# Optimization experiments

Measured on AMD Instinct MI355X. Metric: run time of the kernel, lower is better.

## Reference

```python
import jax, jax.numpy as jnp
import numpy as np

D_MODEL = 1024
N_HEADS = 16
D_V = D_MODEL // N_HEADS  # 64; o_proj maps d_model -> d_v (quirk of the source)
B, S = 4, 2048


def setup_inputs() -> dict:
    key = jax.random.key(0)
    ks = jax.random.split(key, 5)
    scale = 1.0 / np.sqrt(D_MODEL)
    return {
        "in_features": jax.random.normal(ks[0], (B, S, D_MODEL), dtype=jnp.float32),
        "Wq": jax.random.normal(ks[1], (D_MODEL, D_MODEL), dtype=jnp.float32) * scale,
        "Wk": jax.random.normal(ks[2], (D_MODEL, D_MODEL), dtype=jnp.float32) * scale,
        "Wv": jax.random.normal(ks[3], (D_MODEL, D_MODEL), dtype=jnp.float32) * scale,
        "Wo": jax.random.normal(ks[4], (D_V, D_MODEL), dtype=jnp.float32) * scale,
    }


def reference(in_features, Wq, Wk, Wv, Wo):
    # Linear(in, out): y = x @ W^T, no bias. NOTE: source never splits heads;
    # attention runs single-head over the full d_model dims.
    Q = jnp.einsum('bsd,ed->bse', in_features, Wq)  # [B,S,D]
    K = jnp.einsum('bsd,ed->bse', in_features, Wk)
    V = jnp.einsum('bsd,ed->bse', in_features, Wv)

    scores = jnp.einsum('bqd,bkd->bqk', Q, K)       # [B,S,S]
    causal = jnp.tril(jnp.ones((S, S), dtype=bool))  # True = keep
    # source applies -inf mask BEFORE scaling (equivalent result)
    scores = jnp.where(causal[None, :, :], scores, -jnp.inf)
    scores = scores / jnp.sqrt(jnp.float32(D_MODEL))  # K.size(-1) == d_model
    attn = jax.nn.softmax(scores, axis=-1)
    ctx = jnp.einsum('bqk,bkd->bqd', attn, V)        # [B,S,D]
    return jnp.einsum('bsd,vd->bsv', ctx, Wo)        # [B,S,D_V]
```

## Files before the change

### kernel.cpp

```cpp
#include <hip/hip_runtime.h>
#include <math.h>

typedef unsigned short u16;
typedef unsigned int u32;
typedef __attribute__((ext_vector_type(8))) short short8;
typedef __attribute__((ext_vector_type(4))) short short4v;
typedef __attribute__((ext_vector_type(4))) float f32x4;

#define BB 4
#define SS 2048
#define DD 1024
#define DV 64
#define NYU 1152
#define BS (BB * SS)
#define SCALE (1.0f / 32.0f)

__device__ __forceinline__ u16 f2bf(float f) {
    u32 u = __builtin_bit_cast(u32, f);
    u32 r = u + 0x7fffu + ((u >> 16) & 1u);
    return (u16)(r >> 16);
}
__device__ __forceinline__ float bf2f(u16 b) {
    return __builtin_bit_cast(float, (u32)b << 16);
}
__device__ __forceinline__ void storeC(float* p, float v) { *p = v; }
__device__ __forceinline__ void storeC(u16* p, float v) { *p = f2bf(v); }

__global__ __launch_bounds__(256) void prep(const float* __restrict__ x,
                                            const float* __restrict__ Wq,
                                            const float* __restrict__ Wk,
                                            const float* __restrict__ Wo,
                                            const float* __restrict__ Wv,
                                            u16* __restrict__ x16,
                                            u16* __restrict__ Wqt,
                                            u16* __restrict__ Wkt,
                                            float* __restrict__ wpart,
                                            float* __restrict__ out,
                                            float* __restrict__ Lacc) {
    __shared__ float smem[64 * 128];
    const int b = blockIdx.x;
    const int tid = threadIdx.x;
    if (b < 64) {
        const int bb = b;
        const int echunk = (bb & 7) * 128;
        const int kc = bb >> 3, kbase = kc * 128;
        for (int idx = tid; idx < 64 * 128; idx += 256)
            smem[idx] = Wo[(size_t)(idx >> 7) * DD + kbase + (idx & 127)];
        __syncthreads();
        const int eo = echunk + (tid & 31) * 4;
        const int ob = (tid >> 5) * 8;
        float acc[8][4] = {};
        for (int k = 0; k < 128; ++k) {
            f32x4 wv = *(const f32x4*)&Wv[(size_t)(kbase + k) * DD + eo];
#pragma unroll
            for (int oi = 0; oi < 8; ++oi) {
                float s = smem[(ob + oi) * 128 + k];
                acc[oi][0] += s * wv.x; acc[oi][1] += s * wv.y;
                acc[oi][2] += s * wv.z; acc[oi][3] += s * wv.w;
            }
        }
#pragma unroll
        for (int oi = 0; oi < 8; ++oi)
            *(f32x4*)&wpart[((size_t)kc * 64 + ob + oi) * DD + eo] =
                (f32x4){acc[oi][0], acc[oi][1], acc[oi][2], acc[oi][3]};
    } else if (b < 576) {
        const int bb = b - 64;
        const float* src = (bb >> 8) ? Wk : Wq;
        u16* dst = (bb >> 8) ? Wkt : Wqt;
        const int rem = bb & 255;
        const int e0 = (rem >> 4) * 64, d0 = (rem & 15) * 64;
        u16* t = (u16*)smem;
        const int g = tid >> 6, lane = tid & 63;
        for (int r = g; r < 64; r += 4)
            t[r * 72 + lane] = f2bf(src[(size_t)(e0 + r) * DD + d0 + lane]);
        __syncthreads();
        for (int r = g; r < 64; r += 4)
            dst[(size_t)(d0 + r) * DD + e0 + lane] = t[lane * 72 + r];
    } else if (b < 8768) {
        int i = (b - 576) * 256 + tid;
        f32x4 v = ((const f32x4*)x)[i];
        short4v o;
        o.x = (short)f2bf(v.x); o.y = (short)f2bf(v.y);
        o.z = (short)f2bf(v.z); o.w = (short)f2bf(v.w);
        ((short4v*)x16)[i] = o;
    } else if (b < 9280) {
        int i = (b - 8768) * 256 + tid;
        ((f32x4*)out)[i] = (f32x4){0.f, 0.f, 0.f, 0.f};
    } else {
        int i = (b - 9280) * 256 + tid;
        ((f32x4*)Lacc)[i] = (f32x4){0.f, 0.f, 0.f, 0.f};
    }
}

__global__ __launch_bounds__(256) void reduce_all(const float* __restrict__ Gpart,
                                                  const float* __restrict__ wpart,
                                                  u16* __restrict__ Wall2) {
    const int bx = blockIdx.x;
    const int e0 = threadIdx.x * 4;
    f32x4 s = (f32x4){0.f, 0.f, 0.f, 0.f};
    if (bx < 1024) {
#pragma unroll
        for (int kc = 0; kc < 4; ++kc)
            s += *(const f32x4*)&Gpart[(size_t)kc * DD * DD + (size_t)bx * DD + e0];
    } else {
#pragma unroll
        for (int kc = 0; kc < 8; ++kc)
            s += *(const f32x4*)&wpart[((size_t)kc * 64 + bx - 1024) * DD + e0];
    }
    short4v ov;
    ov.x = (short)f2bf(s.x); ov.y = (short)f2bf(s.y);
    ov.z = (short)f2bf(s.z); ov.w = (short)f2bf(s.w);
    *(short4v*)&Wall2[(size_t)bx * DD + e0] = ov;
}

template <int TM, int TN, int WM, int WN, typename OutT, int MODE>
__global__ __launch_bounds__(WM * WN * 64) void gemm_nt_mfma(
    const u16* __restrict__ A, const u16* __restrict__ B, OutT* __restrict__ C,
    int lda, int ldb, int ldc, int K, long sA, long sB, long sC,
    u16* __restrict__ Utp) {
    constexpr int NW = WM * WN;
    constexpr int CA = TM / 16;
    constexpr int CB = TN / 16;
    constexpr int RT = TM / WM;
    constexpr int CT = TN / WN;
    constexpr int AI = RT / 16;
    constexpr int AJ = CT / 16;

    const int z = blockIdx.z;
    A += (size_t)z * sA;
    B += (size_t)z * sB;
    C += (size_t)z * sC;
    int m0, n0;
    if constexpr (MODE == 3) {
        const int b = blockIdx.x;
        const int r = b & 7, q = b >> 3;
        constexpr int RPX = 8192 / TM / 8;
        constexpr int NP = 1152 / TN;
        m0 = (r * RPX + q / NP) * TM;
        n0 = (q % NP) * TN;
    } else {
        m0 = blockIdx.y * TM;
        n0 = blockIdx.x * TN;
    }

    __shared__ u16 As[2][TM * 32];
    __shared__ u16 Bs[2][TN * 32];

    const int tid = threadIdx.x;
    const int w = tid >> 6, lane = tid & 63;
    const int wm = w / WN, wn = w % WN;
    const int lrow = lane >> 2;
    const int lcolsw = (((lane & 3) ^ ((lrow >> 1) & 3)) << 3);
    const int m16 = lane & 15;
    const int rdo = (((lane >> 4) ^ ((m16 >> 1) & 3)) << 3);

    f32x4 acc[AI][AJ];
#pragma unroll
    for (int i = 0; i < AI; ++i)
#pragma unroll
        for (int j = 0; j < AJ; ++j) acc[i][j] = (f32x4){0.f, 0.f, 0.f, 0.f};

    auto stage = [&](int t, int bufi) {
        const int k0 = t * 32;
        for (int c = w; c < CA; c += NW) {
            const u16* g = A + (size_t)(m0 + c * 16 + lrow) * lda + k0 + lcolsw;
            __builtin_amdgcn_global_load_lds(
                (const __attribute__((address_space(1))) void*)g,
                (__attribute__((address_space(3))) void*)(&As[bufi][c * 512]), 16, 0, 0);
        }
        for (int c = w; c < CB; c += NW) {
            const u16* g = B + (size_t)(n0 + c * 16 + lrow) * ldb + k0 + lcolsw;
            __builtin_amdgcn_global_load_lds(
                (const __attribute__((address_space(1))) void*)g,
                (__attribute__((address_space(3))) void*)(&Bs[bufi][c * 512]), 16, 0, 0);
        }
    };

    const int nk = K >> 5;
    stage(0, 0);
    asm volatile("s_waitcnt vmcnt(0)" ::: "memory");
    __syncthreads();

    int cur = 0;
    for (int t = 0; t < nk; ++t) {
        if (t + 1 < nk) stage(t + 1, cur ^ 1);

        short8 a[AI], b[AJ];
#pragma unroll
        for (int i = 0; i < AI; ++i)
            a[i] = *(const short8*)&As[cur][(wm * RT + i * 16 + m16) * 32 + rdo];
#pragma unroll
        for (int j = 0; j < AJ; ++j)
            b[j] = *(const short8*)&Bs[cur][(wn * CT + j * 16 + m16) * 32 + rdo];
#pragma unroll
        for (int i = 0; i < AI; ++i)
#pragma unroll
            for (int j = 0; j < AJ; ++j)
                acc[i][j] = __builtin_amdgcn_mfma_f32_16x16x32_bf16(a[i], b[j], acc[i][j], 0, 0, 0);

        if (t + 1 < nk) {
            asm volatile("s_waitcnt vmcnt(0)" ::: "memory");
            __syncthreads();
        }
        cur ^= 1;
    }

    const int crow0 = m0 + wm * RT + (lane >> 4) * 4;
    const int ccol0 = n0 + wn * CT + m16;
#pragma unroll
    for (int i = 0; i < AI; ++i)
#pragma unroll
        for (int j = 0; j < AJ; ++j)
#pragma unroll
            for (int r = 0; r < 4; ++r) {
                const float v = acc[i][j][r];
                storeC(&C[(size_t)(crow0 + i * 16 + r) * ldc + ccol0 + j * 16], v);
                if constexpr (MODE == 3) {
                    if (n0 + wn * CT == 1024)
                        Utp[(size_t)(ccol0 + j * 16 - 1024) * BS + crow0 + i * 16 + r] = f2bf(v);
                }
            }
}

__global__ __launch_bounds__(128) void scores_pv(const u16* __restrict__ YU,
                                                 const u16* __restrict__ x16,
                                                 const u16* __restrict__ Ut,
                                                 float* __restrict__ out,
                                                 float* __restrict__ Lacc) {
    const int b = blockIdx.x;
    const int r8 = b & 7;
    const int z = r8 >> 1;
    const int t = 2 * (b >> 3) + (r8 & 1);
    auto cum = [](int yy) { int h = yy >> 1; return (yy & 1) ? (h + 1) * (h + 1) : h * (h + 1); };
    int y = (int)(2.0f * sqrtf((float)t + 0.25f));
    if (y > 31) y = 31;
    while (y < 31 && cum(y + 1) <= t) ++y;
    while (y > 0 && cum(y) > t) --y;
    const int m0 = y * 64;
    const int n0 = (t - cum(y)) * 128;

    const u16* A = YU + (size_t)z * SS * NYU;
    const u16* B = x16 + (size_t)z * SS * DD;

    __shared__ union ShU {
        struct { u16 As[2][64 * 32]; u16 Bs[2][128 * 32]; } s;
        u16 Ps[64 * 136];
    } sh;

    const int tid = threadIdx.x;
    const int w = tid >> 6, lane = tid & 63;
    const int lrow = lane >> 2;
    const int lcolsw = (((lane & 3) ^ ((lrow >> 1) & 3)) << 3);
    const int m16 = lane & 15;
    const int kh = (lane >> 4) * 8;
    const int rdo = (((lane >> 4) ^ ((m16 >> 1) & 3)) << 3);

    f32x4 acc[4][4];
#pragma unroll
    for (int i = 0; i < 4; ++i)
#pragma unroll
        for (int j = 0; j < 4; ++j) acc[i][j] = (f32x4){0.f, 0.f, 0.f, 0.f};

    auto stage = [&](int tt, int bufi) {
        const int k0 = tt * 32;
        for (int c = w; c < 4; c += 2) {
            const u16* g = A + (size_t)(m0 + c * 16 + lrow) * NYU + k0 + lcolsw;
            __builtin_amdgcn_global_load_lds(
                (const __attribute__((address_space(1))) void*)g,
                (__attribute__((address_space(3))) void*)(&sh.s.As[bufi][c * 512]), 16, 0, 0);
        }
        for (int c = w; c < 8; c += 2) {
            const u16* g = B + (size_t)(n0 + c * 16 + lrow) * DD + k0 + lcolsw;
            __builtin_amdgcn_global_load_lds(
                (const __attribute__((address_space(1))) void*)g,
                (__attribute__((address_space(3))) void*)(&sh.s.Bs[bufi][c * 512]), 16, 0, 0);
        }
    };

    stage(0, 0);
    asm volatile("s_waitcnt vmcnt(0)" ::: "memory");
    __syncthreads();

    int cur = 0;
    for (int tt = 0; tt < 32; ++tt) {
        if (tt + 1 < 32) stage(tt + 1, cur ^ 1);

        short8 a[4], bb[4];
#pragma unroll
        for (int i = 0; i < 4; ++i)
            a[i] = *(const short8*)&sh.s.As[cur][(i * 16 + m16) * 32 + rdo];
#pragma unroll
        for (int j = 0; j < 4; ++j)
            bb[j] = *(const short8*)&sh.s.Bs[cur][(w * 64 + j * 16 + m16) * 32 + rdo];
#pragma unroll
        for (int i = 0; i < 4; ++i)
#pragma unroll
            for (int j = 0; j < 4; ++j)
                acc[i][j] = __builtin_amdgcn_mfma_f32_16x16x32_bf16(a[i], bb[j], acc[i][j], 0, 0, 0);

        if (tt + 1 < 32) {
            asm volatile("s_waitcnt vmcnt(0)" ::: "memory");
            __syncthreads();
        }
        cur ^= 1;
    }
    __syncthreads();

    const int rl0 = (lane >> 4) * 4;
    const int cl0 = w * 64 + m16;
#pragma unroll
    for (int i = 0; i < 4; ++i)
#pragma unroll
        for (int j = 0; j < 4; ++j)
#pragma unroll
            for (int r = 0; r < 4; ++r) {
                const int rl = rl0 + i * 16 + r;
                const int cl = cl0 + j * 16;
                float p = __expf(acc[i][j][r] * SCALE);
                sh.Ps[rl * 136 + cl] = (n0 + cl <= m0 + rl) ? f2bf(p) : (u16)0;
            }
    __syncthreads();

    short8 ones8;
#pragma unroll
    for (int e = 0; e < 8; ++e) ones8[e] = (short)0x3F80;

    const u16* Utz = Ut + (size_t)z * SS + n0;
    f32x4 accO[2][4], accL[2];
#pragma unroll
    for (int i = 0; i < 2; ++i) {
        accL[i] = (f32x4){0.f, 0.f, 0.f, 0.f};
#pragma unroll
        for (int j = 0; j < 4; ++j) accO[i][j] = (f32x4){0.f, 0.f, 0.f, 0.f};
    }
#pragma unroll
    for (int ks = 0; ks < 4; ++ks) {
        const int k0 = ks * 32;
        short8 a[2], bb[4];
#pragma unroll
        for (int i = 0; i < 2; ++i)
            a[i] = *(const short8*)&sh.Ps[(w * 32 + i * 16 + m16) * 136 + k0 + kh];
#pragma unroll
        for (int j = 0; j < 4; ++j)
            bb[j] = *(const short8*)&Utz[(size_t)(j * 16 + m16) * BS + k0 + kh];
#pragma unroll
        for (int i = 0; i < 2; ++i) {
#pragma unroll
            for (int j = 0; j < 4; ++j)
                accO[i][j] = __builtin_amdgcn_mfma_f32_16x16x32_bf16(a[i], bb[j], accO[i][j], 0, 0, 0);
            accL[i] = __builtin_amdgcn_mfma_f32_16x16x32_bf16(a[i], ones8, accL[i], 0, 0, 0);
        }
    }

    float* Oz = out + (size_t)z * SS * DV;
    float* Lz = Lacc + (size_t)z * SS;
    const int wrow = m0 + w * 32 + (lane >> 4) * 4;
#pragma unroll
    for (int i = 0; i < 2; ++i) {
#pragma unroll
        for (int j = 0; j < 4; ++j)
#pragma unroll
            for (int r = 0; r < 4; ++r)
                atomicAdd(&Oz[(size_t)(wrow + i * 16 + r) * DV + j * 16 + m16],
                          accO[i][j][r]);
        if (m16 == 0)
#pragma unroll
            for (int r = 0; r < 4; ++r)
                atomicAdd(&Lz[wrow + i * 16 + r], accL[i][r]);
    }
}

__global__ __launch_bounds__(256) void normalize(float* __restrict__ out,
                                                 const float* __restrict__ Lacc) {
    int i = blockIdx.x * 256 + threadIdx.x;
    f32x4 v = ((f32x4*)out)[i];
    const float inv = 1.f / Lacc[(i * 4) >> 6];
    v.x *= inv; v.y *= inv; v.z *= inv; v.w *= inv;
    ((f32x4*)out)[i] = v;
}

extern "C" void kernel_launch(void* const* d_in, const int* in_sizes, int n_in,
                              void* d_out, int out_size, void* d_ws, size_t ws_size,
                              hipStream_t stream) {
    const float* x  = (const float*)d_in[0];
    const float* Wq = (const float*)d_in[1];
    const float* Wk = (const float*)d_in[2];
    const float* Wv = (const float*)d_in[3];
    const float* Wo = (const float*)d_in[4];
    float* out = (float*)d_out;

    u16* x16   = (u16*)d_ws;
    u16* Wqt16 = x16 + (size_t)BB * SS * DD;
    u16* Wkt16 = Wqt16 + (size_t)DD * DD;
    u16* Wall2 = Wkt16 + (size_t)DD * DD;
    u16* YU    = Wall2 + (size_t)NYU * DD;
    u16* Ut    = YU + (size_t)BB * SS * NYU;
    float* wpart = (float*)(Ut + (size_t)DV * BS);
    float* Lacc  = wpart + (size_t)8 * 64 * DD;
    float* Gpart = (float*)YU;

    prep<<<dim3(9288), 256, 0, stream>>>(x, Wq, Wk, Wo, Wv, x16, Wqt16, Wkt16,
                                         wpart, out, Lacc);

    gemm_nt_mfma<64, 64, 2, 2, float, 0><<<dim3(16, 16, 4), 256, 0, stream>>>(
        Wkt16, Wqt16, Gpart, DD, DD, DD, 256, 256, 256, (long)DD * DD, nullptr);

    reduce_all<<<dim3(1088), 256, 0, stream>>>(Gpart, wpart, Wall2);

    gemm_nt_mfma<64, 128, 1, 2, u16, 3><<<dim3(1152), 128, 0, stream>>>(
        x16, Wall2, YU, DD, DD, NYU, DD, 0, 0, 0, Ut);

    scores_pv<<<dim3(1088), 128, 0, stream>>>(YU, x16, Ut, out, Lacc);

    normalize<<<dim3(out_size / 4 / 256), 256, 0, stream>>>(out, Lacc);
}
```

Baseline: 200.0 us.

## Fuse YU projection GEMM and causal scores kernel with flag-based dataflow sync

Merges the YU/Ut projection GEMM and the causal scores+PV kernel into one persistent-style launch. Producer blocks signal per-panel completion through global atomic flags, and consumer blocks spin until their row and column panels are ready, so the two stages can overlap. Both stages also move to 128x128 tiles with 256 threads, which halves the scores grid to 544 triangular tiles. The gains sought are removing a kernel boundary and tail idle time. In exchange it relies on producer blocks being scheduled before the consumers that wait on them, and the larger tiles raise register and LDS pressure.

```diff
diff --git a/kernel.cpp b/kernel.cpp
--- a/kernel.cpp
+++ b/kernel.cpp
@@ -14,6 +14,8 @@
 #define NYU 1152
 #define BS (BB * SS)
 #define SCALE (1.0f / 32.0f)
+#define YU_BLOCKS 576
+#define SC_BLOCKS 544
 
 __device__ __forceinline__ u16 f2bf(float f) {
     u32 u = __builtin_bit_cast(u32, f);
@@ -36,7 +38,8 @@
                                             u16* __restrict__ Wkt,
                                             float* __restrict__ wpart,
                                             float* __restrict__ out,
-                                            float* __restrict__ Lacc) {
+                                            float* __restrict__ Lacc,
+                                            int* __restrict__ flags) {
     __shared__ float smem[64 * 128];
     const int b = blockIdx.x;
     const int tid = threadIdx.x;
@@ -86,9 +89,11 @@
     } else if (b < 9280) {
         int i = (b - 8768) * 256 + tid;
         ((f32x4*)out)[i] = (f32x4){0.f, 0.f, 0.f, 0.f};
-    } else {
+    } else if (b < 9288) {
         int i = (b - 9280) * 256 + tid;
         ((f32x4*)Lacc)[i] = (f32x4){0.f, 0.f, 0.f, 0.f};
+    } else {
+        if (tid < 128) flags[tid] = 0;
     }
 }
 
@@ -113,11 +118,10 @@
     *(short4v*)&Wall2[(size_t)bx * DD + e0] = ov;
 }
 
-template <int TM, int TN, int WM, int WN, typename OutT, int MODE>
+template <int TM, int TN, int WM, int WN, typename OutT>
 __global__ __launch_bounds__(WM * WN * 64) void gemm_nt_mfma(
     const u16* __restrict__ A, const u16* __restrict__ B, OutT* __restrict__ C,
-    int lda, int ldb, int ldc, int K, long sA, long sB, long sC,
-    u16* __restrict__ Utp) {
+    int lda, int ldb, int ldc, int K, long sA, long sB, long sC) {
     constexpr int NW = WM * WN;
     constexpr int CA = TM / 16;
     constexpr int CB = TN / 16;
@@ -130,18 +134,8 @@
     A += (size_t)z * sA;
     B += (size_t)z * sB;
     C += (size_t)z * sC;
-    int m0, n0;
-    if constexpr (MODE == 3) {
-        const int b = blockIdx.x;
-        const int r = b & 7, q = b >> 3;
-        constexpr int RPX = 8192 / TM / 8;
-        constexpr int NP = 1152 / TN;
-        m0 = (r * RPX + q / NP) * TM;
-        n0 = (q % NP) * TN;
-    } else {
-        m0 = blockIdx.y * TM;
-        n0 = blockIdx.x * TN;
-    }
+    const int m0 = blockIdx.y * TM;
+    const int n0 = blockIdx.x * TN;
 
     __shared__ u16 As[2][TM * 32];
     __shared__ u16 Bs[2][TN * 32];
@@ -212,161 +206,238 @@
 #pragma unroll
         for (int j = 0; j < AJ; ++j)
 #pragma unroll
-            for (int r = 0; r < 4; ++r) {
-                const float v = acc[i][j][r];
-                storeC(&C[(size_t)(crow0 + i * 16 + r) * ldc + ccol0 + j * 16], v);
-                if constexpr (MODE == 3) {
-                    if (n0 + wn * CT == 1024)
-                        Utp[(size_t)(ccol0 + j * 16 - 1024) * BS + crow0 + i * 16 + r] = f2bf(v);
-                }
-            }
-}
-
-__global__ __launch_bounds__(128) void scores_pv(const u16* __restrict__ YU,
-                                                 const u16* __restrict__ x16,
-                                                 const u16* __restrict__ Ut,
-                                                 float* __restrict__ out,
-                                                 float* __restrict__ Lacc) {
-    const int b = blockIdx.x;
-    const int r8 = b & 7;
-    const int z = r8 >> 1;
-    const int t = 2 * (b >> 3) + (r8 & 1);
-    auto cum = [](int yy) { int h = yy >> 1; return (yy & 1) ? (h + 1) * (h + 1) : h * (h + 1); };
-    int y = (int)(2.0f * sqrtf((float)t + 0.25f));
-    if (y > 31) y = 31;
-    while (y < 31 && cum(y + 1) <= t) ++y;
-    while (y > 0 && cum(y) > t) --y;
-    const int m0 = y * 64;
-    const int n0 = (t - cum(y)) * 128;
-
-    const u16* A = YU + (size_t)z * SS * NYU;
-    const u16* B = x16 + (size_t)z * SS * DD;
-
+            for (int r = 0; r < 4; ++r)
+                storeC(&C[(size_t)(crow0 + i * 16 + r) * ldc + ccol0 + j * 16], acc[i][j][r]);
+}
+
+__global__ __launch_bounds__(256, 4) void yu_scores(
+    const u16* __restrict__ x16, const u16* __restrict__ Wall2,
+    u16* __restrict__ YU, u16* __restrict__ Ut,
+    float* __restrict__ out, float* __restrict__ Lacc,
+    int* __restrict__ flags) {
     __shared__ union ShU {
-        struct { u16 As[2][64 * 32]; u16 Bs[2][128 * 32]; } s;
-        u16 Ps[64 * 136];
+        struct { u16 As[2][128 * 32]; u16 Bs[2][128 * 32]; } s;
+        u16 Ps[128 * 136];
     } sh;
 
     const int tid = threadIdx.x;
     const int w = tid >> 6, lane = tid & 63;
+    const int wm = w >> 1, wn = w & 1;
     const int lrow = lane >> 2;
     const int lcolsw = (((lane & 3) ^ ((lrow >> 1) & 3)) << 3);
     const int m16 = lane & 15;
     const int kh = (lane >> 4) * 8;
     const int rdo = (((lane >> 4) ^ ((m16 >> 1) & 3)) << 3);
 
-    f32x4 acc[4][4];
-#pragma unroll
-    for (int i = 0; i < 4; ++i)
-#pragma unroll
-        for (int j = 0; j < 4; ++j) acc[i][j] = (f32x4){0.f, 0.f, 0.f, 0.f};
-
-    auto stage = [&](int tt, int bufi) {
-        const int k0 = tt * 32;
-        for (int c = w; c < 4; c += 2) {
-            const u16* g = A + (size_t)(m0 + c * 16 + lrow) * NYU + k0 + lcolsw;
-            __builtin_amdgcn_global_load_lds(
-                (const __attribute__((address_space(1))) void*)g,
-                (__attribute__((address_space(3))) void*)(&sh.s.As[bufi][c * 512]), 16, 0, 0);
-        }
-        for (int c = w; c < 8; c += 2) {
-            const u16* g = B + (size_t)(n0 + c * 16 + lrow) * DD + k0 + lcolsw;
-            __builtin_amdgcn_global_load_lds(
-                (const __attribute__((address_space(1))) void*)g,
-                (__attribute__((address_space(3))) void*)(&sh.s.Bs[bufi][c * 512]), 16, 0, 0);
-        }
-    };
-
-    stage(0, 0);
-    asm volatile("s_waitcnt vmcnt(0)" ::: "memory");
-    __syncthreads();
-
-    int cur = 0;
-    for (int tt = 0; tt < 32; ++tt) {
-        if (tt + 1 < 32) stage(tt + 1, cur ^ 1);
-
-        short8 a[4], bb[4];
+    if (blockIdx.x < YU_BLOCKS) {
+        const int b = blockIdx.x;
+        const int r = b & 7, q = b >> 3;
+        const int m0 = (r * 8 + q / 9) * 128;
+        const int n0 = (q % 9) * 128;
+
+        f32x4 acc[4][4];
 #pragma unroll
         for (int i = 0; i < 4; ++i)
-            a[i] = *(const short8*)&sh.s.As[cur][(i * 16 + m16) * 32 + rdo];
-#pragma unroll
-        for (int j = 0; j < 4; ++j)
-            bb[j] = *(const short8*)&sh.s.Bs[cur][(w * 64 + j * 16 + m16) * 32 + rdo];
+#pragma unroll
+            for (int j = 0; j < 4; ++j) acc[i][j] = (f32x4){0.f, 0.f, 0.f, 0.f};
+
+        auto stage = [&](int t, int bufi) {
+            const int k0 = t * 32;
+            for (int c = w; c < 8; c += 4) {
+                const u16* g = x16 + (size_t)(m0 + c * 16 + lrow) * DD + k0 + lcolsw;
+                __builtin_amdgcn_global_load_lds(
+                    (const __attribute__((address_space(1))) void*)g,
+                    (__attribute__((address_space(3))) void*)(&sh.s.As[bufi][c * 512]), 16, 0, 0);
+            }
+            for (int c = w; c < 8; c += 4) {
+                const u16* g = Wall2 + (size_t)(n0 + c * 16 + lrow) * DD + k0 + lcolsw;
+                __builtin_amdgcn_global_load_lds(
+                    (const __attribute__((address_space(1))) void*)g,
+                    (__attribute__((address_space(3))) void*)(&sh.s.Bs[bufi][c * 512]), 16, 0, 0);
+            }
+        };
+
+        stage(0, 0);
+        asm volatile("s_waitcnt vmcnt(0)" ::: "memory");
+        __syncthreads();
+        int cur = 0;
+        for (int t = 0; t < 32; ++t) {
+            if (t + 1 < 32) stage(t + 1, cur ^ 1);
+            short8 a[4], bb[4];
+#pragma unroll
+            for (int i = 0; i < 4; ++i)
+                a[i] = *(const short8*)&sh.s.As[cur][(wm * 64 + i * 16 + m16) * 32 + rdo];
+#pragma unroll
+            for (int j = 0; j < 4; ++j)
+                bb[j] = *(const short8*)&sh.s.Bs[cur][(wn * 64 + j * 16 + m16) * 32 + rdo];
+#pragma unroll
+            for (int i = 0; i < 4; ++i)
+#pragma unroll
+                for (int j = 0; j < 4; ++j)
+                    acc[i][j] = __builtin_amdgcn_mfma_f32_16x16x32_bf16(a[i], bb[j], acc[i][j], 0, 0, 0);
+            if (t + 1 < 32) {
+                asm volatile("s_waitcnt vmcnt(0)" ::: "memory");
+                __syncthreads();
+            }
+            cur ^= 1;
+        }
+
+        const int crow0 = m0 + wm * 64 + (lane >> 4) * 4;
+        const int ccol0 = n0 + wn * 64 + m16;
 #pragma unroll
         for (int i = 0; i < 4; ++i)
 #pragma unroll
             for (int j = 0; j < 4; ++j)
-                acc[i][j] = __builtin_amdgcn_mfma_f32_16x16x32_bf16(a[i], bb[j], acc[i][j], 0, 0, 0);
-
-        if (tt + 1 < 32) {
-            asm volatile("s_waitcnt vmcnt(0)" ::: "memory");
-            __syncthreads();
-        }
-        cur ^= 1;
-    }
-    __syncthreads();
-
-    const int rl0 = (lane >> 4) * 4;
-    const int cl0 = w * 64 + m16;
-#pragma unroll
-    for (int i = 0; i < 4; ++i)
-#pragma unroll
-        for (int j = 0; j < 4; ++j)
-#pragma unroll
-            for (int r = 0; r < 4; ++r) {
-                const int rl = rl0 + i * 16 + r;
-                const int cl = cl0 + j * 16;
-                float p = __expf(acc[i][j][r] * SCALE);
-                sh.Ps[rl * 136 + cl] = (n0 + cl <= m0 + rl) ? f2bf(p) : (u16)0;
-            }
-    __syncthreads();
-
-    short8 ones8;
-#pragma unroll
-    for (int e = 0; e < 8; ++e) ones8[e] = (short)0x3F80;
-
-    const u16* Utz = Ut + (size_t)z * SS + n0;
-    f32x4 accO[2][4], accL[2];
-#pragma unroll
-    for (int i = 0; i < 2; ++i) {
-        accL[i] = (f32x4){0.f, 0.f, 0.f, 0.f};
-#pragma unroll
-        for (int j = 0; j < 4; ++j) accO[i][j] = (f32x4){0.f, 0.f, 0.f, 0.f};
-    }
-#pragma unroll
-    for (int ks = 0; ks < 4; ++ks) {
-        const int k0 = ks * 32;
-        short8 a[2], bb[4];
-#pragma unroll
-        for (int i = 0; i < 2; ++i)
-            a[i] = *(const short8*)&sh.Ps[(w * 32 + i * 16 + m16) * 136 + k0 + kh];
-#pragma unroll
-        for (int j = 0; j < 4; ++j)
-            bb[j] = *(const short8*)&Utz[(size_t)(j * 16 + m16) * BS + k0 + kh];
+#pragma unroll
+                for (int r = 0; r < 4; ++r) {
+                    const float v = acc[i][j][r];
+                    YU[(size_t)(crow0 + i * 16 + r) * NYU + ccol0 + j * 16] = f2bf(v);
+                    if (n0 == 1024 && wn == 0)
+                        Ut[(size_t)(ccol0 + j * 16 - 1024) * BS + crow0 + i * 16 + r] = f2bf(v);
+                }
+        __threadfence();
+        __syncthreads();
+        if (tid == 0) {
+            const int panel = m0 >> 7;
+            if (n0 == 1024)
+                __hip_atomic_store(&flags[64 + panel], 1, __ATOMIC_RELEASE, __HIP_MEMORY_SCOPE_AGENT);
+            else
+                __hip_atomic_fetch_add(&flags[panel], 1, __ATOMIC_RELEASE, __HIP_MEMORY_SCOPE_AGENT);
+        }
+    } else {
+        const int b = blockIdx.x - YU_BLOCKS;
+        const int r8 = b & 7;
+        const int z = r8 >> 1;
+        const int t = 2 * (b >> 3) + (r8 & 1);
+        int y = (int)((sqrtf(8.f * t + 1.f) - 1.f) * 0.5f);
+        while ((y + 1) * (y + 2) / 2 <= t) ++y;
+        while (y * (y + 1) / 2 > t) --y;
+        const int m0 = y * 128;
+        const int c = t - y * (y + 1) / 2;
+        const int n0 = c * 128;
+
+        if (tid == 0) {
+            const int gy = z * 16 + y, gc = z * 16 + c;
+            while (__hip_atomic_load(&flags[gy], __ATOMIC_ACQUIRE, __HIP_MEMORY_SCOPE_AGENT) < 8)
+                __builtin_amdgcn_s_sleep(8);
+            while (__hip_atomic_load(&flags[64 + gc], __ATOMIC_ACQUIRE, __HIP_MEMORY_SCOPE_AGENT) == 0)
+                __builtin_amdgcn_s_sleep(8);
+        }
+        __syncthreads();
+
+        const u16* A = YU + (size_t)z * SS * NYU;
+        const u16* B = x16 + (size_t)z * SS * DD;
+
+        f32x4 acc[4][4];
+#pragma unroll
+        for (int i = 0; i < 4; ++i)
+#pragma unroll
+            for (int j = 0; j < 4; ++j) acc[i][j] = (f32x4){0.f, 0.f, 0.f, 0.f};
+
+        auto stage = [&](int tt, int bufi) {
+            const int k0 = tt * 32;
+            for (int cc = w; cc < 8; cc += 4) {
+                const u16* g = A + (size_t)(m0 + cc * 16 + lrow) * NYU + k0 + lcolsw;
+                __builtin_amdgcn_global_load_lds(
+                    (const __attribute__((address_space(1))) void*)g,
+                    (__attribute__((address_space(3))) void*)(&sh.s.As[bufi][cc * 512]), 16, 0, 0);
+            }
+            for (int cc = w; cc < 8; cc += 4) {
+                const u16* g = B + (size_t)(n0 + cc * 16 + lrow) * DD + k0 + lcolsw;
+                __builtin_amdgcn_global_load_lds(
+                    (const __attribute__((address_space(1))) void*)g,
+                    (__attribute__((address_space(3))) void*)(&sh.s.Bs[bufi][cc * 512]), 16, 0, 0);
+            }
+        };
+
+        stage(0, 0);
+        asm volatile("s_waitcnt vmcnt(0)" ::: "memory");
+        __syncthreads();
+        int cur = 0;
+        for (int tt = 0; tt < 32; ++tt) {
+            if (tt + 1 < 32) stage(tt + 1, cur ^ 1);
+            short8 a[4], bb[4];
+#pragma unroll
+            for (int i = 0; i < 4; ++i)
+                a[i] = *(const short8*)&sh.s.As[cur][(wm * 64 + i * 16 + m16) * 32 + rdo];
+#pragma unroll
+            for (int j = 0; j < 4; ++j)
+                bb[j] = *(const short8*)&sh.s.Bs[cur][(wn * 64 + j * 16 + m16) * 32 + rdo];
+#pragma unroll
+            for (int i = 0; i < 4; ++i)
+#pragma unroll
+                for (int j = 0; j < 4; ++j)
+                    acc[i][j] = __builtin_amdgcn_mfma_f32_16x16x32_bf16(a[i], bb[j], acc[i][j], 0, 0, 0);
+            if (tt + 1 < 32) {
+                asm volatile("s_waitcnt vmcnt(0)" ::: "memory");
+                __syncthreads();
+            }
+            cur ^= 1;
+        }
+        __syncthreads();
+
+        const int rl0 = wm * 64 + (lane >> 4) * 4;
+        const int cl0 = wn * 64 + m16;
+#pragma unroll
+        for (int i = 0; i < 4; ++i)
+#pragma unroll
+            for (int j = 0; j < 4; ++j)
+#pragma unroll
+                for (int r = 0; r < 4; ++r) {
+                    const int rl = rl0 + i * 16 + r;
+                    const int cl = cl0 + j * 16;
+                    float p = __expf(acc[i][j][r] * SCALE);
+                    sh.Ps[rl * 136 + cl] = (n0 + cl <= m0 + rl) ? f2bf(p) : (u16)0;
+                }
+        __syncthreads();
+
+        short8 ones8;
+#pragma unroll
+        for (int e = 0; e < 8; ++e) ones8[e] = (short)0x3F80;
+
+        const u16* Utz = Ut + (size_t)z * SS + n0;
+        f32x4 accO[2][4], accL[2];
 #pragma unroll
         for (int i = 0; i < 2; ++i) {
-#pragma unroll
-            for (int j = 0; j < 4; ++j)
-                accO[i][j] = __builtin_amdgcn_mfma_f32_16x16x32_bf16(a[i], bb[j], accO[i][j], 0, 0, 0);
-            accL[i] = __builtin_amdgcn_mfma_f32_16x16x32_bf16(a[i], ones8, accL[i], 0, 0, 0);
-        }
-    }
-
-    float* Oz = out + (size_t)z * SS * DV;
-    float* Lz = Lacc + (size_t)z * SS;
-    const int wrow = m0 + w * 32 + (lane >> 4) * 4;
-#pragma unroll
-    for (int i = 0; i < 2; ++i) {
-#pragma unroll
-        for (int j = 0; j < 4; ++j)
-#pragma unroll
-            for (int r = 0; r < 4; ++r)
-                atomicAdd(&Oz[(size_t)(wrow + i * 16 + r) * DV + j * 16 + m16],
-                          accO[i][j][r]);
-        if (m16 == 0)
-#pragma unroll
-            for (int r = 0; r < 4; ++r)
-                atomicAdd(&Lz[wrow + i * 16 + r], accL[i][r]);
+            accL[i] = (f32x4){0.f, 0.f, 0.f, 0.f};
+#pragma unroll
+            for (int j = 0; j < 4; ++j) accO[i][j] = (f32x4){0.f, 0.f, 0.f, 0.f};
+        }
+#pragma unroll
+        for (int ks = 0; ks < 4; ++ks) {
+            const int k0 = ks * 32;
+            short8 a[2], bb[4];
+#pragma unroll
+            for (int i = 0; i < 2; ++i)
+                a[i] = *(const short8*)&sh.Ps[(w * 32 + i * 16 + m16) * 136 + k0 + kh];
+#pragma unroll
+            for (int j = 0; j < 4; ++j)
+                bb[j] = *(const short8*)&Utz[(size_t)(j * 16 + m16) * BS + k0 + kh];
+#pragma unroll
+            for (int i = 0; i < 2; ++i) {
+#pragma unroll
+                for (int j = 0; j < 4; ++j)
+                    accO[i][j] = __builtin_amdgcn_mfma_f32_16x16x32_bf16(a[i], bb[j], accO[i][j], 0, 0, 0);
+                accL[i] = __builtin_amdgcn_mfma_f32_16x16x32_bf16(a[i], ones8, accL[i], 0, 0, 0);
+            }
+        }
+
+        float* Oz = out + (size_t)z * SS * DV;
+        float* Lz = Lacc + (size_t)z * SS;
+        const int wrow = m0 + w * 32 + (lane >> 4) * 4;
+#pragma unroll
+        for (int i = 0; i < 2; ++i) {
+#pragma unroll
+            for (int j = 0; j < 4; ++j)
+#pragma unroll
+                for (int r = 0; r < 4; ++r)
+                    atomicAdd(&Oz[(size_t)(wrow + i * 16 + r) * DV + j * 16 + m16],
+                              accO[i][j][r]);
+            if (m16 == 0)
+#pragma unroll
+                for (int r = 0; r < 4; ++r)
+                    atomicAdd(&Lz[wrow + i * 16 + r], accL[i][r]);
+        }
     }
 }
 
@@ -397,20 +468,19 @@
     u16* Ut    = YU + (size_t)BB * SS * NYU;
     float* wpart = (float*)(Ut + (size_t)DV * BS);
     float* Lacc  = wpart + (size_t)8 * 64 * DD;
+    int* flags   = (int*)(Lacc + (size_t)BB * SS);
     float* Gpart = (float*)YU;
 
-    prep<<<dim3(9288), 256, 0, stream>>>(x, Wq, Wk, Wo, Wv, x16, Wqt16, Wkt16,
-                                         wpart, out, Lacc);
-
-    gemm_nt_mfma<64, 64, 2, 2, float, 0><<<dim3(16, 16, 4), 256, 0, stream>>>(
-        Wkt16, Wqt16, Gpart, DD, DD, DD, 256, 256, 256, (long)DD * DD, nullptr);
+    prep<<<dim3(9289), 256, 0, stream>>>(x, Wq, Wk, Wo, Wv, x16, Wqt16, Wkt16,
+                                         wpart, out, Lacc, flags);
+
+    gemm_nt_mfma<64, 64, 2, 2, float><<<dim3(16, 16, 4), 256, 0, stream>>>(
+        Wkt16, Wqt16, Gpart, DD, DD, DD, 256, 256, 256, (long)DD * DD);
 
     reduce_all<<<dim3(1088), 256, 0, stream>>>(Gpart, wpart, Wall2);
 
-    gemm_nt_mfma<64, 128, 1, 2, u16, 3><<<dim3(1152), 128, 0, stream>>>(
-        x16, Wall2, YU, DD, DD, NYU, DD, 0, 0, 0, Ut);
-
-    scores_pv<<<dim3(1088), 128, 0, stream>>>(YU, x16, Ut, out, Lacc);
+    yu_scores<<<dim3(YU_BLOCKS + SC_BLOCKS), 256, 0, stream>>>(
+        x16, Wall2, YU, Ut, out, Lacc, flags);
 
     normalize<<<dim3(out_size / 4 / 256), 256, 0, stream>>>(out, Lacc);
 }
```

After: 443.3 us. +121.7%, slower.

## Split-K the YU projection GEMM and enlarge tiles in scores kernel

Applied to the files above, without the earlier changes.

The x·Wall GEMM moves to 128x128 tiles with four waves. When the workspace is large enough, it also splits K in two, writing two bf16 partial outputs (YU/Y1 and Ut/Ut1), which doubles the grid to 1152 blocks for better occupancy. The scores_pv kernel moves to 128x128 causal tiles with four waves and 544 blocks, and sums the two partials inside its MFMA loops. The trade-off is extra workspace traffic, doubled A-loads and MFMAs in the scores stage, and slight extra rounding from the bf16 partials.

```diff
diff --git a/kernel.cpp b/kernel.cpp
--- a/kernel.cpp
+++ b/kernel.cpp
@@ -113,11 +113,11 @@
     *(short4v*)&Wall2[(size_t)bx * DD + e0] = ov;
 }
 
-template <int TM, int TN, int WM, int WN, typename OutT, int MODE>
+template <int TM, int TN, int WM, int WN, typename OutT, int MODE, int NS>
 __global__ __launch_bounds__(WM * WN * 64) void gemm_nt_mfma(
     const u16* __restrict__ A, const u16* __restrict__ B, OutT* __restrict__ C,
     int lda, int ldb, int ldc, int K, long sA, long sB, long sC,
-    u16* __restrict__ Utp) {
+    OutT* __restrict__ C1, u16* __restrict__ Utp, u16* __restrict__ Utp1) {
     constexpr int NW = WM * WN;
     constexpr int CA = TM / 16;
     constexpr int CB = TN / 16;
@@ -130,14 +130,16 @@
     A += (size_t)z * sA;
     B += (size_t)z * sB;
     C += (size_t)z * sC;
-    int m0, n0;
+    int m0, n0, kc = 0;
     if constexpr (MODE == 3) {
         const int b = blockIdx.x;
-        const int r = b & 7, q = b >> 3;
+        const int r = b & 7;
+        int q = b >> 3;
+        if constexpr (NS == 2) { kc = q & 1; q >>= 1; }
         constexpr int RPX = 8192 / TM / 8;
-        constexpr int NP = 1152 / TN;
-        m0 = (r * RPX + q / NP) * TM;
-        n0 = (q % NP) * TN;
+        m0 = (r * RPX + q / 9) * TM;
+        n0 = (q % 9) * TN;
+        if (kc) { C = C1; Utp = Utp1; }
     } else {
         m0 = blockIdx.y * TM;
         n0 = blockIdx.x * TN;
@@ -176,14 +178,15 @@
         }
     };
 
-    const int nk = K >> 5;
-    stage(0, 0);
+    const int tb = kc * (K / NS) / 32;
+    const int te = (kc + 1) * (K / NS) / 32;
+    stage(tb, 0);
     asm volatile("s_waitcnt vmcnt(0)" ::: "memory");
     __syncthreads();
 
     int cur = 0;
-    for (int t = 0; t < nk; ++t) {
-        if (t + 1 < nk) stage(t + 1, cur ^ 1);
+    for (int t = tb; t < te; ++t) {
+        if (t + 1 < te) stage(t + 1, cur ^ 1);
 
         short8 a[AI], b[AJ];
 #pragma unroll
@@ -198,7 +201,7 @@
             for (int j = 0; j < AJ; ++j)
                 acc[i][j] = __builtin_amdgcn_mfma_f32_16x16x32_bf16(a[i], b[j], acc[i][j], 0, 0, 0);
 
-        if (t + 1 < nk) {
+        if (t + 1 < te) {
             asm volatile("s_waitcnt vmcnt(0)" ::: "memory");
             __syncthreads();
         }
@@ -216,39 +219,42 @@
                 const float v = acc[i][j][r];
                 storeC(&C[(size_t)(crow0 + i * 16 + r) * ldc + ccol0 + j * 16], v);
                 if constexpr (MODE == 3) {
-                    if (n0 + wn * CT == 1024)
+                    if (n0 == 1024 && wn == 0)
                         Utp[(size_t)(ccol0 + j * 16 - 1024) * BS + crow0 + i * 16 + r] = f2bf(v);
                 }
             }
 }
 
-__global__ __launch_bounds__(128) void scores_pv(const u16* __restrict__ YU,
+__global__ __launch_bounds__(256) void scores_pv(const u16* __restrict__ YU,
                                                  const u16* __restrict__ x16,
                                                  const u16* __restrict__ Ut,
+                                                 const u16* __restrict__ YU1,
+                                                 const u16* __restrict__ Ut1,
+                                                 int split,
                                                  float* __restrict__ out,
                                                  float* __restrict__ Lacc) {
     const int b = blockIdx.x;
     const int r8 = b & 7;
     const int z = r8 >> 1;
     const int t = 2 * (b >> 3) + (r8 & 1);
-    auto cum = [](int yy) { int h = yy >> 1; return (yy & 1) ? (h + 1) * (h + 1) : h * (h + 1); };
-    int y = (int)(2.0f * sqrtf((float)t + 0.25f));
-    if (y > 31) y = 31;
-    while (y < 31 && cum(y + 1) <= t) ++y;
-    while (y > 0 && cum(y) > t) --y;
-    const int m0 = y * 64;
-    const int n0 = (t - cum(y)) * 128;
-
-    const u16* A = YU + (size_t)z * SS * NYU;
+    int y = (int)((sqrtf(8.f * t + 1.f) - 1.f) * 0.5f);
+    while ((y + 1) * (y + 2) / 2 <= t) ++y;
+    while (y * (y + 1) / 2 > t) --y;
+    const int m0 = y * 128;
+    const int n0 = (t - y * (y + 1) / 2) * 128;
+
+    const u16* A0 = YU + (size_t)z * SS * NYU;
+    const u16* A1 = YU1 + (size_t)z * SS * NYU;
     const u16* B = x16 + (size_t)z * SS * DD;
 
     __shared__ union ShU {
-        struct { u16 As[2][64 * 32]; u16 Bs[2][128 * 32]; } s;
-        u16 Ps[64 * 136];
+        struct { u16 As0[2][128 * 32]; u16 As1[2][128 * 32]; u16 Bs[2][128 * 32]; } s;
+        u16 Ps[128 * 136];
     } sh;
 
     const int tid = threadIdx.x;
     const int w = tid >> 6, lane = tid & 63;
+    const int wm = w >> 1, wn = w & 1;
     const int lrow = lane >> 2;
     const int lcolsw = (((lane & 3) ^ ((lrow >> 1) & 3)) << 3);
     const int m16 = lane & 15;
@@ -263,13 +269,21 @@
 
     auto stage = [&](int tt, int bufi) {
         const int k0 = tt * 32;
-        for (int c = w; c < 4; c += 2) {
-            const u16* g = A + (size_t)(m0 + c * 16 + lrow) * NYU + k0 + lcolsw;
+        for (int c = w; c < 8; c += 4) {
+            const u16* g = A0 + (size_t)(m0 + c * 16 + lrow) * NYU + k0 + lcolsw;
             __builtin_amdgcn_global_load_lds(
                 (const __attribute__((address_space(1))) void*)g,
-                (__attribute__((address_space(3))) void*)(&sh.s.As[bufi][c * 512]), 16, 0, 0);
-        }
-        for (int c = w; c < 8; c += 2) {
+                (__attribute__((address_space(3))) void*)(&sh.s.As0[bufi][c * 512]), 16, 0, 0);
+        }
+        if (split) {
+            for (int c = w; c < 8; c += 4) {
+                const u16* g = A1 + (size_t)(m0 + c * 16 + lrow) * NYU + k0 + lcolsw;
+                __builtin_amdgcn_global_load_lds(
+                    (const __attribute__((address_space(1))) void*)g,
+                    (__attribute__((address_space(3))) void*)(&sh.s.As1[bufi][c * 512]), 16, 0, 0);
+            }
+        }
+        for (int c = w; c < 8; c += 4) {
             const u16* g = B + (size_t)(n0 + c * 16 + lrow) * DD + k0 + lcolsw;
             __builtin_amdgcn_global_load_lds(
                 (const __attribute__((address_space(1))) void*)g,
@@ -285,18 +299,29 @@
     for (int tt = 0; tt < 32; ++tt) {
         if (tt + 1 < 32) stage(tt + 1, cur ^ 1);
 
-        short8 a[4], bb[4];
+        short8 a0[4], bb[4];
 #pragma unroll
         for (int i = 0; i < 4; ++i)
-            a[i] = *(const short8*)&sh.s.As[cur][(i * 16 + m16) * 32 + rdo];
+            a0[i] = *(const short8*)&sh.s.As0[cur][(wm * 64 + i * 16 + m16) * 32 + rdo];
 #pragma unroll
         for (int j = 0; j < 4; ++j)
-            bb[j] = *(const short8*)&sh.s.Bs[cur][(w * 64 + j * 16 + m16) * 32 + rdo];
+            bb[j] = *(const short8*)&sh.s.Bs[cur][(wn * 64 + j * 16 + m16) * 32 + rdo];
 #pragma unroll
         for (int i = 0; i < 4; ++i)
 #pragma unroll
             for (int j = 0; j < 4; ++j)
-                acc[i][j] = __builtin_amdgcn_mfma_f32_16x16x32_bf16(a[i], bb[j], acc[i][j], 0, 0, 0);
+                acc[i][j] = __builtin_amdgcn_mfma_f32_16x16x32_bf16(a0[i], bb[j], acc[i][j], 0, 0, 0);
+        if (split) {
+            short8 a1[4];
+#pragma unroll
+            for (int i = 0; i < 4; ++i)
+                a1[i] = *(const short8*)&sh.s.As1[cur][(wm * 64 + i * 16 + m16) * 32 + rdo];
+#pragma unroll
+            for (int i = 0; i < 4; ++i)
+#pragma unroll
+                for (int j = 0; j < 4; ++j)
+                    acc[i][j] = __builtin_amdgcn_mfma_f32_16x16x32_bf16(a1[i], bb[j], acc[i][j], 0, 0, 0);
+        }
 
         if (tt + 1 < 32) {
             asm volatile("s_waitcnt vmcnt(0)" ::: "memory");
@@ -306,8 +331,8 @@
     }
     __syncthreads();
 
-    const int rl0 = (lane >> 4) * 4;
-    const int cl0 = w * 64 + m16;
+    const int rl0 = wm * 64 + (lane >> 4) * 4;
+    const int cl0 = wn * 64 + m16;
 #pragma unroll
     for (int i = 0; i < 4; ++i)
 #pragma unroll
@@ -325,7 +350,8 @@
 #pragma unroll
     for (int e = 0; e < 8; ++e) ones8[e] = (short)0x3F80;
 
-    const u16* Utz = Ut + (size_t)z * SS + n0;
+    const u16* Ut0z = Ut + (size_t)z * SS + n0;
+    const u16* Ut1z = Ut1 + (size_t)z * SS + n0;
     f32x4 accO[2][4], accL[2];
 #pragma unroll
     for (int i = 0; i < 2; ++i) {
@@ -336,19 +362,30 @@
 #pragma unroll
     for (int ks = 0; ks < 4; ++ks) {
         const int k0 = ks * 32;
-        short8 a[2], bb[4];
+        short8 a[2], bb0[4];
 #pragma unroll
         for (int i = 0; i < 2; ++i)
             a[i] = *(const short8*)&sh.Ps[(w * 32 + i * 16 + m16) * 136 + k0 + kh];
 #pragma unroll
         for (int j = 0; j < 4; ++j)
-            bb[j] = *(const short8*)&Utz[(size_t)(j * 16 + m16) * BS + k0 + kh];
+            bb0[j] = *(const short8*)&Ut0z[(size_t)(j * 16 + m16) * BS + k0 + kh];
 #pragma unroll
         for (int i = 0; i < 2; ++i) {
 #pragma unroll
             for (int j = 0; j < 4; ++j)
-                accO[i][j] = __builtin_amdgcn_mfma_f32_16x16x32_bf16(a[i], bb[j], accO[i][j], 0, 0, 0);
+                accO[i][j] = __builtin_amdgcn_mfma_f32_16x16x32_bf16(a[i], bb0[j], accO[i][j], 0, 0, 0);
             accL[i] = __builtin_amdgcn_mfma_f32_16x16x32_bf16(a[i], ones8, accL[i], 0, 0, 0);
+        }
+        if (split) {
+            short8 bb1[4];
+#pragma unroll
+            for (int j = 0; j < 4; ++j)
+                bb1[j] = *(const short8*)&Ut1z[(size_t)(j * 16 + m16) * BS + k0 + kh];
+#pragma unroll
+            for (int i = 0; i < 2; ++i)
+#pragma unroll
+                for (int j = 0; j < 4; ++j)
+                    accO[i][j] = __builtin_amdgcn_mfma_f32_16x16x32_bf16(a[i], bb1[j], accO[i][j], 0, 0, 0);
         }
     }
 
@@ -397,20 +434,30 @@
     u16* Ut    = YU + (size_t)BB * SS * NYU;
     float* wpart = (float*)(Ut + (size_t)DV * BS);
     float* Lacc  = wpart + (size_t)8 * 64 * DD;
+    u16* Y1    = (u16*)(Lacc + (size_t)BB * SS);
+    u16* Ut1   = Y1 + (size_t)BB * SS * NYU;
     float* Gpart = (float*)YU;
+
+    const size_t need = (size_t)((char*)(Ut1 + (size_t)DV * BS) - (char*)d_ws);
+    const int split = (ws_size >= need) ? 1 : 0;
 
     prep<<<dim3(9288), 256, 0, stream>>>(x, Wq, Wk, Wo, Wv, x16, Wqt16, Wkt16,
                                          wpart, out, Lacc);
 
-    gemm_nt_mfma<64, 64, 2, 2, float, 0><<<dim3(16, 16, 4), 256, 0, stream>>>(
-        Wkt16, Wqt16, Gpart, DD, DD, DD, 256, 256, 256, (long)DD * DD, nullptr);
+    gemm_nt_mfma<64, 64, 2, 2, float, 0, 1><<<dim3(16, 16, 4), 256, 0, stream>>>(
+        Wkt16, Wqt16, Gpart, DD, DD, DD, 256, 256, 256, (long)DD * DD,
+        nullptr, nullptr, nullptr);
 
     reduce_all<<<dim3(1088), 256, 0, stream>>>(Gpart, wpart, Wall2);
 
-    gemm_nt_mfma<64, 128, 1, 2, u16, 3><<<dim3(1152), 128, 0, stream>>>(
-        x16, Wall2, YU, DD, DD, NYU, DD, 0, 0, 0, Ut);
-
-    scores_pv<<<dim3(1088), 128, 0, stream>>>(YU, x16, Ut, out, Lacc);
+    if (split)
+        gemm_nt_mfma<128, 128, 2, 2, u16, 3, 2><<<dim3(1152), 256, 0, stream>>>(
+            x16, Wall2, YU, DD, DD, NYU, DD, 0, 0, 0, Y1, Ut, Ut1);
+    else
+        gemm_nt_mfma<128, 128, 2, 2, u16, 3, 1><<<dim3(576), 256, 0, stream>>>(
+            x16, Wall2, YU, DD, DD, NYU, DD, 0, 0, 0, nullptr, Ut, nullptr);
+
+    scores_pv<<<dim3(544), 256, 0, stream>>>(YU, x16, Ut, Y1, Ut1, split, out, Lacc);
 
     normalize<<<dim3(out_size / 4 / 256), 256, 0, stream>>>(out, Lacc);
 }
```

Measured after the change: 230.7 us. 15.4% more time.
